# Performance work log

Measured on AMD Instinct MI355X. Metric: run time of the kernel, lower is better.

## Reference

```python
import jax, jax.numpy as jnp
import numpy as np

B, S, HID = 4, 1024, 1024
NH = 32
HD = HID // NH  # 32, equals NH (required by the module's bias broadcast)
MAX_POS = 1024
EPS = 1e-12


def setup_inputs() -> dict:
    key = jax.random.key(0)
    ks = jax.random.split(key, 12)
    sc = 0.02
    return {
        "hidden_states": jax.random.normal(ks[0], (B, S, HID), jnp.float32),
        "Wq": jax.random.normal(ks[1], (HID, HID), jnp.float32) * sc,
        "bq": jnp.zeros((HID,), jnp.float32),
        "Wk": jax.random.normal(ks[2], (HID, HID), jnp.float32) * sc,
        "bk": jnp.zeros((HID,), jnp.float32),
        "Wv": jax.random.normal(ks[3], (HID, HID), jnp.float32) * sc,
        "bv": jnp.zeros((HID,), jnp.float32),
        "Wo": jax.random.normal(ks[4], (HID, HID), jnp.float32) * sc,
        "bo": jnp.zeros((HID,), jnp.float32),
        "ln_gamma": jnp.ones((HID,), jnp.float32),
        "ln_beta": jnp.zeros((HID,), jnp.float32),
        "dist_emb": jax.random.normal(ks[5], (2 * MAX_POS - 1, HD), jnp.float32) * sc,
    }


def reference(hidden_states, Wq, bq, Wk, bk, Wv, bv, Wo, bo, ln_gamma, ln_beta, dist_emb):
    b, s, hid = hidden_states.shape
    # QKV projections (torch Linear: x @ W.T + b), split heads -> (b, h, s, d)
    def split_heads(x):
        return x.reshape(b, s, NH, HD).transpose(0, 2, 1, 3)
    q = split_heads(hidden_states @ Wq.T + bq)
    k = split_heads(hidden_states @ Wk.T + bk)
    v = split_heads(hidden_states @ Wv.T + bv)

    # Relative position bias: rel in [0, 2*max_pos-2], emb -> (s, s, HD)
    pos = jnp.arange(s)
    rel = pos[:, None] - pos[None, :] + (MAX_POS - 1)  # (s, s)
    # permute(0,3,1,2): (b, HD, s, s); identical across batch -> broadcast.
    # Broadcasts against (b, NH, s, s) since HD == NH (module requirement).
    bias = dist_emb[rel].transpose(2, 0, 1)  # (HD, s, s)

    scores = jnp.einsum("bhqd,bhkd->bhqk", q, k)  # (b, h, s, s)
    scores = (scores + bias[None]) / np.sqrt(HD)  # bias added BEFORE scaling, as in source
    probs = jax.nn.softmax(scores, axis=-1)

    ctx = jnp.einsum("bhqk,bhkd->bhqd", probs, v)
    ctx = ctx.transpose(0, 2, 1, 3).reshape(b, s, hid)
    attn_out = ctx @ Wo.T + bo

    # residual + LayerNorm
    x = attn_out + hidden_states
    mu = jnp.mean(x, axis=-1, keepdims=True)
    var = jnp.mean(jnp.square(x - mu), axis=-1, keepdims=True)
    out = (x - mu) / jnp.sqrt(var + EPS) * ln_gamma + ln_beta
    return out, probs
```

## Files before the change

### kernel.cpp

```cpp
#include <hip/hip_runtime.h>
#include <math.h>

#define BB 4
#define SS 1024
#define HIDD 1024
#define NH 32
#define HD 32
#define RS 0.17677669529663687f

#define BM 128
#define BN 128
#define BK 16

__global__ __launch_bounds__(256) void gemm_qkv(
    const float* __restrict__ X,
    const float* __restrict__ W0, const float* __restrict__ W1, const float* __restrict__ W2,
    const float* __restrict__ c0, const float* __restrict__ c1, const float* __restrict__ c2,
    float* __restrict__ O0, float* __restrict__ O1, float* __restrict__ O2)
{
    const int zi = blockIdx.z;
    const float* Wm = (zi == 0) ? W0 : (zi == 1 ? W1 : W2);
    const float* bm = (zi == 0) ? c0 : (zi == 1 ? c1 : c2);
    float* Om       = (zi == 0) ? O0 : (zi == 1 ? O1 : O2);

    const int i0 = blockIdx.x * BM;
    const int j0 = blockIdx.y * BN;
    const int tid = threadIdx.x;
    const int tx = tid & 15, ty = tid >> 4;
    const int m0 = tx * 8, n0 = ty * 8;

    __shared__ float As[BK][BM + 4];
    __shared__ float Bs[BK][BN + 4];

    float acc[8][8] = {};

    for (int k0 = 0; k0 < 1024; k0 += BK) {
        #pragma unroll
        for (int f0 = 0; f0 < 2; ++f0) {
            int f = tid + f0 * 256;
            int r = f >> 2;
            int c4 = (f & 3) * 4;
            float4 a = *(const float4*)&X[(size_t)(i0 + r) * 1024 + k0 + c4];
            As[c4 + 0][r] = a.x; As[c4 + 1][r] = a.y;
            As[c4 + 2][r] = a.z; As[c4 + 3][r] = a.w;
            float4 w = *(const float4*)&Wm[(size_t)(j0 + r) * 1024 + k0 + c4];
            Bs[c4 + 0][r] = w.x; Bs[c4 + 1][r] = w.y;
            Bs[c4 + 2][r] = w.z; Bs[c4 + 3][r] = w.w;
        }
        __syncthreads();
        #pragma unroll
        for (int k = 0; k < BK; ++k) {
            float ar[8], br[8];
            *(float4*)&ar[0] = *(const float4*)&As[k][m0];
            *(float4*)&ar[4] = *(const float4*)&As[k][m0 + 4];
            *(float4*)&br[0] = *(const float4*)&Bs[k][n0];
            *(float4*)&br[4] = *(const float4*)&Bs[k][n0 + 4];
            #pragma unroll
            for (int mm = 0; mm < 8; ++mm)
                #pragma unroll
                for (int nn = 0; nn < 8; ++nn)
                    acc[mm][nn] += ar[mm] * br[nn];
        }
        __syncthreads();
    }

    #pragma unroll
    for (int mm = 0; mm < 8; ++mm) {
        int i = i0 + m0 + mm;
        int bi = i >> 10, si = i & 1023;
        #pragma unroll
        for (int nn4 = 0; nn4 < 8; nn4 += 4) {
            int j = j0 + n0 + nn4;
            int h = j >> 5, d = j & 31;
            float4 o;
            o.x = acc[mm][nn4 + 0] + bm[j + 0];
            o.y = acc[mm][nn4 + 1] + bm[j + 1];
            o.z = acc[mm][nn4 + 2] + bm[j + 2];
            o.w = acc[mm][nn4 + 3] + bm[j + 3];
            *(float4*)&Om[(((size_t)bi * NH + h) * SS + si) * HD + d] = o;
        }
    }
}

__global__ __launch_bounds__(256) void gemm_out(
    const float* __restrict__ X, const float* __restrict__ Wm,
    const float* __restrict__ bm, const float* __restrict__ res,
    float* __restrict__ Om)
{
    const int i0 = blockIdx.x * BM;
    const int j0 = blockIdx.y * BN;
    const int tid = threadIdx.x;
    const int tx = tid & 15, ty = tid >> 4;
    const int m0 = tx * 8, n0 = ty * 8;

    __shared__ float As[BK][BM + 4];
    __shared__ float Bs[BK][BN + 4];

    float acc[8][8] = {};

    for (int k0 = 0; k0 < 1024; k0 += BK) {
        #pragma unroll
        for (int f0 = 0; f0 < 2; ++f0) {
            int f = tid + f0 * 256;
            int r = f >> 2;
            int c4 = (f & 3) * 4;
            float4 a = *(const float4*)&X[(size_t)(i0 + r) * 1024 + k0 + c4];
            As[c4 + 0][r] = a.x; As[c4 + 1][r] = a.y;
            As[c4 + 2][r] = a.z; As[c4 + 3][r] = a.w;
            float4 w = *(const float4*)&Wm[(size_t)(j0 + r) * 1024 + k0 + c4];
            Bs[c4 + 0][r] = w.x; Bs[c4 + 1][r] = w.y;
            Bs[c4 + 2][r] = w.z; Bs[c4 + 3][r] = w.w;
        }
        __syncthreads();
        #pragma unroll
        for (int k = 0; k < BK; ++k) {
            float ar[8], br[8];
            *(float4*)&ar[0] = *(const float4*)&As[k][m0];
            *(float4*)&ar[4] = *(const float4*)&As[k][m0 + 4];
            *(float4*)&br[0] = *(const float4*)&Bs[k][n0];
            *(float4*)&br[4] = *(const float4*)&Bs[k][n0 + 4];
            #pragma unroll
            for (int mm = 0; mm < 8; ++mm)
                #pragma unroll
                for (int nn = 0; nn < 8; ++nn)
                    acc[mm][nn] += ar[mm] * br[nn];
        }
        __syncthreads();
    }

    #pragma unroll
    for (int mm = 0; mm < 8; ++mm) {
        int i = i0 + m0 + mm;
        #pragma unroll
        for (int nn4 = 0; nn4 < 8; nn4 += 4) {
            int j = j0 + n0 + nn4;
            float4 r4 = *(const float4*)&res[(size_t)i * 1024 + j];
            float4 o;
            o.x = acc[mm][nn4 + 0] + bm[j + 0] + r4.x;
            o.y = acc[mm][nn4 + 1] + bm[j + 1] + r4.y;
            o.z = acc[mm][nn4 + 2] + bm[j + 2] + r4.z;
            o.w = acc[mm][nn4 + 3] + bm[j + 3] + r4.w;
            *(float4*)&Om[(size_t)i * 1024 + j] = o;
        }
    }
}

__global__ __launch_bounds__(256) void attn_kernel(
    const float* __restrict__ Q, const float* __restrict__ K,
    const float* __restrict__ V, const float* __restrict__ dist,
    float* __restrict__ probs, float* __restrict__ ctx)
{
    const int tile = blockIdx.x;
    const int h = blockIdx.y;
    const int b = blockIdx.z;
    const int tid = threadIdx.x;
    const int r0 = tile * 512;
    const size_t bh = (size_t)(b * NH + h);
    const float* Qh = Q + bh * SS * HD;
    const float* Kh = K + bh * SS * HD;
    const float* Vh = V + bh * SS * HD;
    float* Ph = probs + bh * SS * SS;

    __shared__ float Kt[512 * HD];
    __shared__ float Vt[512 * HD];
    __shared__ float dl[1536];

    for (int t = tid; t < 1535; t += 256)
        dl[t] = dist[(size_t)(r0 + t) * HD + h];

    for (int f = tid; f < 4096; f += 256) {
        ((float4*)Kt)[f] = ((const float4*)Kh)[f];
        ((float4*)Vt)[f] = ((const float4*)Kh)[f + 4096];
    }

    float q1[32], q2[32];
    #pragma unroll
    for (int d4 = 0; d4 < 8; ++d4) {
        float4 a = ((const float4*)(Qh + (size_t)(r0 + tid) * HD))[d4];
        q1[d4 * 4 + 0] = a.x; q1[d4 * 4 + 1] = a.y;
        q1[d4 * 4 + 2] = a.z; q1[d4 * 4 + 3] = a.w;
        float4 c = ((const float4*)(Qh + (size_t)(r0 + 256 + tid) * HD))[d4];
        q2[d4 * 4 + 0] = c.x; q2[d4 * 4 + 1] = c.y;
        q2[d4 * 4 + 2] = c.z; q2[d4 * 4 + 3] = c.w;
    }
    __syncthreads();

    float m1 = -1e30f, l1 = 0.f, m2 = -1e30f, l2 = 0.f;
    #pragma unroll 1
    for (int ht = 0; ht < 2; ++ht) {
        const float* KT = ht ? Vt : Kt;
        const int jbase = ht * 512;
        #pragma unroll 2
        for (int j = 0; j < 512; ++j) {
            const float* kr = KT + j * HD;
            float a1 = 0.f, a2 = 0.f;
            #pragma unroll
            for (int d4 = 0; d4 < 8; ++d4) {
                float4 kv = ((const float4*)kr)[d4];
                a1 += q1[d4*4+0]*kv.x + q1[d4*4+1]*kv.y + q1[d4*4+2]*kv.z + q1[d4*4+3]*kv.w;
                a2 += q2[d4*4+0]*kv.x + q2[d4*4+1]*kv.y + q2[d4*4+2]*kv.z + q2[d4*4+3]*kv.w;
            }
            int jg = jbase + j;
            float s1 = (a1 + dl[tid + 1023 - jg]) * RS;
            float s2 = (a2 + dl[tid + 1279 - jg]) * RS;
            if (s1 > m1) { l1 *= __expf(m1 - s1); m1 = s1; }
            l1 += __expf(s1 - m1);
            if (s2 > m2) { l2 *= __expf(m2 - s2); m2 = s2; }
            l2 += __expf(s2 - m2);
        }
    }
    const float rl1 = 1.f / l1, rl2 = 1.f / l2;

    float c1[32] = {}, c2[32] = {};

    #pragma unroll 1
    for (int jt = 0; jt < 2; ++jt) {
        __syncthreads();
        for (int f = tid; f < 4096; f += 256) {
            if (jt) ((float4*)Kt)[f] = ((const float4*)(Kh + (size_t)jt * 512 * HD))[f];
            ((float4*)Vt)[f] = ((const float4*)(Vh + (size_t)jt * 512 * HD))[f];
        }
        __syncthreads();

        #pragma unroll 1
        for (int jj = 0; jj < 512; jj += 4) {
            float pa1[4], pa2[4];
            #pragma unroll
            for (int u = 0; u < 4; ++u) {
                const float* kr = Kt + (jj + u) * HD;
                float a1 = 0.f, a2 = 0.f;
                #pragma unroll
                for (int d4 = 0; d4 < 8; ++d4) {
                    float4 kv = ((const float4*)kr)[d4];
                    a1 += q1[d4*4+0]*kv.x + q1[d4*4+1]*kv.y + q1[d4*4+2]*kv.z + q1[d4*4+3]*kv.w;
                    a2 += q2[d4*4+0]*kv.x + q2[d4*4+1]*kv.y + q2[d4*4+2]*kv.z + q2[d4*4+3]*kv.w;
                }
                int jg = jt * 512 + jj + u;
                float s1 = (a1 + dl[tid + 1023 - jg]) * RS;
                float s2 = (a2 + dl[tid + 1279 - jg]) * RS;
                pa1[u] = __expf(s1 - m1) * rl1;
                pa2[u] = __expf(s2 - m2) * rl2;
            }
            int jg0 = jt * 512 + jj;
            *(float4*)&Ph[(size_t)(r0 + tid) * SS + jg0] =
                make_float4(pa1[0], pa1[1], pa1[2], pa1[3]);
            *(float4*)&Ph[(size_t)(r0 + 256 + tid) * SS + jg0] =
                make_float4(pa2[0], pa2[1], pa2[2], pa2[3]);
            #pragma unroll
            for (int u = 0; u < 4; ++u) {
                const float* vr = Vt + (jj + u) * HD;
                #pragma unroll
                for (int d4 = 0; d4 < 8; ++d4) {
                    float4 vv = ((const float4*)vr)[d4];
                    c1[d4*4+0] += pa1[u]*vv.x; c1[d4*4+1] += pa1[u]*vv.y;
                    c1[d4*4+2] += pa1[u]*vv.z; c1[d4*4+3] += pa1[u]*vv.w;
                    c2[d4*4+0] += pa2[u]*vv.x; c2[d4*4+1] += pa2[u]*vv.y;
                    c2[d4*4+2] += pa2[u]*vv.z; c2[d4*4+3] += pa2[u]*vv.w;
                }
            }
        }
    }

    float* cp1 = ctx + (size_t)(b * SS + r0 + tid) * HIDD + h * HD;
    float* cp2 = ctx + (size_t)(b * SS + r0 + 256 + tid) * HIDD + h * HD;
    #pragma unroll
    for (int d4 = 0; d4 < 8; ++d4) {
        ((float4*)cp1)[d4] = make_float4(c1[d4*4], c1[d4*4+1], c1[d4*4+2], c1[d4*4+3]);
        ((float4*)cp2)[d4] = make_float4(c2[d4*4], c2[d4*4+1], c2[d4*4+2], c2[d4*4+3]);
    }
}

__global__ __launch_bounds__(256) void ln_kernel(
    const float* __restrict__ X, const float* __restrict__ gamma,
    const float* __restrict__ beta, float* __restrict__ out)
{
    const int row = blockIdx.x;
    const int tid = threadIdx.x;
    const float* xr = X + (size_t)row * 1024;
    float4 x = *(const float4*)&xr[tid * 4];
    float s = x.x + x.y + x.z + x.w;
    float q = x.x*x.x + x.y*x.y + x.z*x.z + x.w*x.w;
    #pragma unroll
    for (int off = 32; off; off >>= 1) {
        s += __shfl_xor(s, off);
        q += __shfl_xor(q, off);
    }
    __shared__ float ps[4], pq[4];
    int wid = tid >> 6, lane = tid & 63;
    if (lane == 0) { ps[wid] = s; pq[wid] = q; }
    __syncthreads();
    s = ps[0] + ps[1] + ps[2] + ps[3];
    q = pq[0] + pq[1] + pq[2] + pq[3];
    float mu = s * (1.0f / 1024.0f);
    float var = q * (1.0f / 1024.0f) - mu * mu;
    float rstd = 1.0f / sqrtf(var + 1e-12f);
    float4 g = *(const float4*)&gamma[tid * 4];
    float4 bt = *(const float4*)&beta[tid * 4];
    float4 o;
    o.x = (x.x - mu) * rstd * g.x + bt.x;
    o.y = (x.y - mu) * rstd * g.y + bt.y;
    o.z = (x.z - mu) * rstd * g.z + bt.z;
    o.w = (x.w - mu) * rstd * g.w + bt.w;
    *(float4*)&out[(size_t)row * 1024 + tid * 4] = o;
}

extern "C" void kernel_launch(void* const* d_in, const int* in_sizes, int n_in,
                              void* d_out, int out_size, void* d_ws, size_t ws_size,
                              hipStream_t stream)
{
    const float* hid  = (const float*)d_in[0];
    const float* Wq   = (const float*)d_in[1];
    const float* bq   = (const float*)d_in[2];
    const float* Wk   = (const float*)d_in[3];
    const float* bk   = (const float*)d_in[4];
    const float* Wv   = (const float*)d_in[5];
    const float* bvv  = (const float*)d_in[6];
    const float* Wo   = (const float*)d_in[7];
    const float* bo   = (const float*)d_in[8];
    const float* lng  = (const float*)d_in[9];
    const float* lnb  = (const float*)d_in[10];
    const float* dist = (const float*)d_in[11];

    float* out   = (float*)d_out;
    float* probs = out + (size_t)BB * SS * HIDD;

    const size_t QN = (size_t)BB * NH * SS * HD;
    float* ws   = (float*)d_ws;
    float* Qb   = ws;
    float* Kb   = ws + QN;
    float* Vb   = ws + 2 * QN;
    float* ctxb = ws + 3 * QN;
    float* xres = ws;

    gemm_qkv<<<dim3(32, 8, 3), 256, 0, stream>>>(hid, Wq, Wk, Wv, bq, bk, bvv, Qb, Kb, Vb);
    attn_kernel<<<dim3(2, NH, BB), 256, 0, stream>>>(Qb, Kb, Vb, dist, probs, ctxb);
    gemm_out<<<dim3(32, 8), 256, 0, stream>>>(ctxb, Wo, bo, hid, xres);
    ln_kernel<<<4096, 256, 0, stream>>>(xres, lng, lnb, out);
}
```

Measured before the change: 1.850 ms.

## Retile attention into 32-row query blocks with swizzled LDS and cooperative softmax

The attention kernel is rebuilt so each block handles 32 query rows instead of 512. Each thread computes a 2x8 score micro-tile over 128-key chunks staged in XOR-swizzled LDS. Row max and sum statistics, and the context accumulators, are combined with cross-lane shuffles, which raises the grid from 256 to 4096 blocks and lets each CU hold more blocks at once. Separately, both GEMMs change the per-thread row and column mapping to two strided groups of 4, to reduce LDS bank conflicts on the fragment reads. The costs are extra shuffle reductions over 64 context values per thread and re-staging K and V for every query block.

```diff
diff --git a/kernel.cpp b/kernel.cpp
--- a/kernel.cpp
+++ b/kernel.cpp
@@ -27,7 +27,8 @@
     const int j0 = blockIdx.y * BN;
     const int tid = threadIdx.x;
     const int tx = tid & 15, ty = tid >> 4;
-    const int m0 = tx * 8, n0 = ty * 8;
+    const int ra = tx * 4, rb = 64 + tx * 4;
+    const int ca = ty * 4, cb = 64 + ty * 4;
 
     __shared__ float As[BK][BM + 4];
     __shared__ float Bs[BK][BN + 4];
@@ -51,10 +52,10 @@
         #pragma unroll
         for (int k = 0; k < BK; ++k) {
             float ar[8], br[8];
-            *(float4*)&ar[0] = *(const float4*)&As[k][m0];
-            *(float4*)&ar[4] = *(const float4*)&As[k][m0 + 4];
-            *(float4*)&br[0] = *(const float4*)&Bs[k][n0];
-            *(float4*)&br[4] = *(const float4*)&Bs[k][n0 + 4];
+            *(float4*)&ar[0] = *(const float4*)&As[k][ra];
+            *(float4*)&ar[4] = *(const float4*)&As[k][rb];
+            *(float4*)&br[0] = *(const float4*)&Bs[k][ca];
+            *(float4*)&br[4] = *(const float4*)&Bs[k][cb];
             #pragma unroll
             for (int mm = 0; mm < 8; ++mm)
                 #pragma unroll
@@ -66,17 +67,17 @@
 
     #pragma unroll
     for (int mm = 0; mm < 8; ++mm) {
-        int i = i0 + m0 + mm;
+        int i = i0 + ((mm < 4) ? (ra + mm) : (rb + mm - 4));
         int bi = i >> 10, si = i & 1023;
         #pragma unroll
-        for (int nn4 = 0; nn4 < 8; nn4 += 4) {
-            int j = j0 + n0 + nn4;
+        for (int g = 0; g < 2; ++g) {
+            int j = j0 + (g == 0 ? ca : cb);
             int h = j >> 5, d = j & 31;
             float4 o;
-            o.x = acc[mm][nn4 + 0] + bm[j + 0];
-            o.y = acc[mm][nn4 + 1] + bm[j + 1];
-            o.z = acc[mm][nn4 + 2] + bm[j + 2];
-            o.w = acc[mm][nn4 + 3] + bm[j + 3];
+            o.x = acc[mm][g*4 + 0] + bm[j + 0];
+            o.y = acc[mm][g*4 + 1] + bm[j + 1];
+            o.z = acc[mm][g*4 + 2] + bm[j + 2];
+            o.w = acc[mm][g*4 + 3] + bm[j + 3];
             *(float4*)&Om[(((size_t)bi * NH + h) * SS + si) * HD + d] = o;
         }
     }
@@ -91,7 +92,8 @@
     const int j0 = blockIdx.y * BN;
     const int tid = threadIdx.x;
     const int tx = tid & 15, ty = tid >> 4;
-    const int m0 = tx * 8, n0 = ty * 8;
+    const int ra = tx * 4, rb = 64 + tx * 4;
+    const int ca = ty * 4, cb = 64 + ty * 4;
 
     __shared__ float As[BK][BM + 4];
     __shared__ float Bs[BK][BN + 4];
@@ -115,10 +117,10 @@
         #pragma unroll
         for (int k = 0; k < BK; ++k) {
             float ar[8], br[8];
-            *(float4*)&ar[0] = *(const float4*)&As[k][m0];
-            *(float4*)&ar[4] = *(const float4*)&As[k][m0 + 4];
-            *(float4*)&br[0] = *(const float4*)&Bs[k][n0];
-            *(float4*)&br[4] = *(const float4*)&Bs[k][n0 + 4];
+            *(float4*)&ar[0] = *(const float4*)&As[k][ra];
+            *(float4*)&ar[4] = *(const float4*)&As[k][rb];
+            *(float4*)&br[0] = *(const float4*)&Bs[k][ca];
+            *(float4*)&br[4] = *(const float4*)&Bs[k][cb];
             #pragma unroll
             for (int mm = 0; mm < 8; ++mm)
                 #pragma unroll
@@ -130,143 +132,180 @@
 
     #pragma unroll
     for (int mm = 0; mm < 8; ++mm) {
-        int i = i0 + m0 + mm;
-        #pragma unroll
-        for (int nn4 = 0; nn4 < 8; nn4 += 4) {
-            int j = j0 + n0 + nn4;
+        int i = i0 + ((mm < 4) ? (ra + mm) : (rb + mm - 4));
+        #pragma unroll
+        for (int g = 0; g < 2; ++g) {
+            int j = j0 + (g == 0 ? ca : cb);
             float4 r4 = *(const float4*)&res[(size_t)i * 1024 + j];
             float4 o;
-            o.x = acc[mm][nn4 + 0] + bm[j + 0] + r4.x;
-            o.y = acc[mm][nn4 + 1] + bm[j + 1] + r4.y;
-            o.z = acc[mm][nn4 + 2] + bm[j + 2] + r4.z;
-            o.w = acc[mm][nn4 + 3] + bm[j + 3] + r4.w;
+            o.x = acc[mm][g*4 + 0] + bm[j + 0] + r4.x;
+            o.y = acc[mm][g*4 + 1] + bm[j + 1] + r4.y;
+            o.z = acc[mm][g*4 + 2] + bm[j + 2] + r4.z;
+            o.w = acc[mm][g*4 + 3] + bm[j + 3] + r4.w;
             *(float4*)&Om[(size_t)i * 1024 + j] = o;
         }
     }
 }
 
-__global__ __launch_bounds__(256) void attn_kernel(
+__global__ __launch_bounds__(256, 3) void attn_kernel(
     const float* __restrict__ Q, const float* __restrict__ K,
     const float* __restrict__ V, const float* __restrict__ dist,
     float* __restrict__ probs, float* __restrict__ ctx)
 {
-    const int tile = blockIdx.x;
-    const int h = blockIdx.y;
-    const int b = blockIdx.z;
+    const int q0 = blockIdx.x * 32;
+    const int h  = blockIdx.y;
+    const int b  = blockIdx.z;
     const int tid = threadIdx.x;
-    const int r0 = tile * 512;
+    const int rg = tid >> 4;
+    const int cg = tid & 15;
     const size_t bh = (size_t)(b * NH + h);
     const float* Qh = Q + bh * SS * HD;
     const float* Kh = K + bh * SS * HD;
     const float* Vh = V + bh * SS * HD;
     float* Ph = probs + bh * SS * SS;
 
-    __shared__ float Kt[512 * HD];
-    __shared__ float Vt[512 * HD];
-    __shared__ float dl[1536];
-
-    for (int t = tid; t < 1535; t += 256)
-        dl[t] = dist[(size_t)(r0 + t) * HD + h];
-
-    for (int f = tid; f < 4096; f += 256) {
-        ((float4*)Kt)[f] = ((const float4*)Kh)[f];
-        ((float4*)Vt)[f] = ((const float4*)Kh)[f + 4096];
-    }
-
-    float q1[32], q2[32];
-    #pragma unroll
-    for (int d4 = 0; d4 < 8; ++d4) {
-        float4 a = ((const float4*)(Qh + (size_t)(r0 + tid) * HD))[d4];
-        q1[d4 * 4 + 0] = a.x; q1[d4 * 4 + 1] = a.y;
-        q1[d4 * 4 + 2] = a.z; q1[d4 * 4 + 3] = a.w;
-        float4 c = ((const float4*)(Qh + (size_t)(r0 + 256 + tid) * HD))[d4];
-        q2[d4 * 4 + 0] = c.x; q2[d4 * 4 + 1] = c.y;
-        q2[d4 * 4 + 2] = c.z; q2[d4 * 4 + 3] = c.w;
-    }
-    __syncthreads();
-
-    float m1 = -1e30f, l1 = 0.f, m2 = -1e30f, l2 = 0.f;
-    #pragma unroll 1
-    for (int ht = 0; ht < 2; ++ht) {
-        const float* KT = ht ? Vt : Kt;
-        const int jbase = ht * 512;
-        #pragma unroll 2
-        for (int j = 0; j < 512; ++j) {
-            const float* kr = KT + j * HD;
-            float a1 = 0.f, a2 = 0.f;
+    __shared__ float Qs[32 * 32];
+    __shared__ float Kt[128 * 32];
+    __shared__ float Vt[128 * 32];
+    __shared__ float dl[1055];
+
+    {
+        int r = tid >> 3, d4 = tid & 7;
+        float4 qv = *(const float4*)&Qh[(size_t)(q0 + r) * HD + d4 * 4];
+        *(float4*)&Qs[r * 32 + ((d4 ^ (r & 7)) << 2)] = qv;
+        for (int t = tid; t < 1055; t += 256)
+            dl[t] = dist[(size_t)(q0 + t) * HD + h];
+    }
+
+    auto stage = [&](float* lds, const float* src, int c0) {
+        #pragma unroll
+        for (int it = 0; it < 4; ++it) {
+            int f4 = tid + it * 256;
+            int c = f4 >> 3;
+            int d4 = f4 & 7;
+            float4 v = *(const float4*)&src[(size_t)(c0 + c) * HD + d4 * 4];
+            *(float4*)&lds[c * 32 + ((d4 ^ ((c >> 3) & 7)) << 2)] = v;
+        }
+    };
+
+    const int r0l = rg * 2, r1l = rg * 2 + 1;
+
+    auto qk_tile = [&](const float* Kb, int c0, float sv[2][8]) {
+        #pragma unroll
+        for (int i = 0; i < 2; ++i)
+            #pragma unroll
+            for (int u = 0; u < 8; ++u) sv[i][u] = 0.f;
+        #pragma unroll
+        for (int d4 = 0; d4 < 8; ++d4) {
+            float4 qa = *(const float4*)&Qs[r0l * 32 + ((d4 ^ (r0l & 7)) << 2)];
+            float4 qb = *(const float4*)&Qs[r1l * 32 + ((d4 ^ (r1l & 7)) << 2)];
+            #pragma unroll
+            for (int u = 0; u < 8; ++u) {
+                const int cl = ((u >> 2) << 6) + (cg << 2) + (u & 3);
+                float4 kv = *(const float4*)&Kb[cl * 32 + ((d4 ^ ((cl >> 3) & 7)) << 2)];
+                sv[0][u] += qa.x*kv.x + qa.y*kv.y + qa.z*kv.z + qa.w*kv.w;
+                sv[1][u] += qb.x*kv.x + qb.y*kv.y + qb.z*kv.z + qb.w*kv.w;
+            }
+        }
+        #pragma unroll
+        for (int i = 0; i < 2; ++i)
+            #pragma unroll
+            for (int u = 0; u < 8; ++u) {
+                const int cl = ((u >> 2) << 6) + (cg << 2) + (u & 3);
+                sv[i][u] = (sv[i][u] + dl[r0l + i + 1023 - c0 - cl]) * RS;
+            }
+    };
+
+    float mr[2] = {-1e30f, -1e30f}, lr[2] = {0.f, 0.f};
+
+    auto ml_update = [&](float sv[2][8]) {
+        #pragma unroll
+        for (int i = 0; i < 2; ++i) {
+            float tm = sv[i][0];
+            #pragma unroll
+            for (int u = 1; u < 8; ++u) tm = fmaxf(tm, sv[i][u]);
+            float M = fmaxf(mr[i], tm);
+            lr[i] *= __expf(mr[i] - M);
+            mr[i] = M;
+            #pragma unroll
+            for (int u = 0; u < 8; ++u) lr[i] += __expf(sv[i][u] - M);
+        }
+    };
+
+    for (int t = 0; t < 8; t += 2) {
+        __syncthreads();
+        stage(Kt, Kh, t * 128);
+        stage(Vt, Kh, (t + 1) * 128);
+        __syncthreads();
+        float sv[2][8];
+        qk_tile(Kt, t * 128, sv);       ml_update(sv);
+        qk_tile(Vt, (t + 1) * 128, sv); ml_update(sv);
+    }
+
+    #pragma unroll
+    for (int off = 1; off < 16; off <<= 1) {
+        #pragma unroll
+        for (int i = 0; i < 2; ++i) {
+            float mo = __shfl_xor(mr[i], off);
+            float lo = __shfl_xor(lr[i], off);
+            float M = fmaxf(mr[i], mo);
+            lr[i] = lr[i] * __expf(mr[i] - M) + lo * __expf(mo - M);
+            mr[i] = M;
+        }
+    }
+    const float rl0 = 1.f / lr[0], rl1 = 1.f / lr[1];
+
+    float ca0[32] = {}, ca1[32] = {};
+    for (int t = 0; t < 8; ++t) {
+        const int c0 = t * 128;
+        __syncthreads();
+        stage(Kt, Kh, c0);
+        stage(Vt, Vh, c0);
+        __syncthreads();
+        float sv[2][8];
+        qk_tile(Kt, c0, sv);
+        float p0[8], p1[8];
+        #pragma unroll
+        for (int u = 0; u < 8; ++u) {
+            p0[u] = __expf(sv[0][u] - mr[0]) * rl0;
+            p1[u] = __expf(sv[1][u] - mr[1]) * rl1;
+        }
+        #pragma unroll
+        for (int u4 = 0; u4 < 2; ++u4) {
+            int cbase = c0 + u4 * 64 + (cg << 2);
+            *(float4*)&Ph[(size_t)(q0 + r0l) * SS + cbase] =
+                make_float4(p0[u4*4+0], p0[u4*4+1], p0[u4*4+2], p0[u4*4+3]);
+            *(float4*)&Ph[(size_t)(q0 + r1l) * SS + cbase] =
+                make_float4(p1[u4*4+0], p1[u4*4+1], p1[u4*4+2], p1[u4*4+3]);
+        }
+        #pragma unroll
+        for (int u = 0; u < 8; ++u) {
+            const int cl = ((u >> 2) << 6) + (cg << 2) + (u & 3);
+            const float pa = p0[u], pb = p1[u];
             #pragma unroll
             for (int d4 = 0; d4 < 8; ++d4) {
-                float4 kv = ((const float4*)kr)[d4];
-                a1 += q1[d4*4+0]*kv.x + q1[d4*4+1]*kv.y + q1[d4*4+2]*kv.z + q1[d4*4+3]*kv.w;
-                a2 += q2[d4*4+0]*kv.x + q2[d4*4+1]*kv.y + q2[d4*4+2]*kv.z + q2[d4*4+3]*kv.w;
+                float4 vv = *(const float4*)&Vt[cl * 32 + ((d4 ^ ((cl >> 3) & 7)) << 2)];
+                ca0[d4*4+0] += pa*vv.x; ca0[d4*4+1] += pa*vv.y;
+                ca0[d4*4+2] += pa*vv.z; ca0[d4*4+3] += pa*vv.w;
+                ca1[d4*4+0] += pb*vv.x; ca1[d4*4+1] += pb*vv.y;
+                ca1[d4*4+2] += pb*vv.z; ca1[d4*4+3] += pb*vv.w;
             }
-            int jg = jbase + j;
-            float s1 = (a1 + dl[tid + 1023 - jg]) * RS;
-            float s2 = (a2 + dl[tid + 1279 - jg]) * RS;
-            if (s1 > m1) { l1 *= __expf(m1 - s1); m1 = s1; }
-            l1 += __expf(s1 - m1);
-            if (s2 > m2) { l2 *= __expf(m2 - s2); m2 = s2; }
-            l2 += __expf(s2 - m2);
-        }
-    }
-    const float rl1 = 1.f / l1, rl2 = 1.f / l2;
-
-    float c1[32] = {}, c2[32] = {};
-
-    #pragma unroll 1
-    for (int jt = 0; jt < 2; ++jt) {
-        __syncthreads();
-        for (int f = tid; f < 4096; f += 256) {
-            if (jt) ((float4*)Kt)[f] = ((const float4*)(Kh + (size_t)jt * 512 * HD))[f];
-            ((float4*)Vt)[f] = ((const float4*)(Vh + (size_t)jt * 512 * HD))[f];
-        }
-        __syncthreads();
-
-        #pragma unroll 1
-        for (int jj = 0; jj < 512; jj += 4) {
-            float pa1[4], pa2[4];
-            #pragma unroll
-            for (int u = 0; u < 4; ++u) {
-                const float* kr = Kt + (jj + u) * HD;
-                float a1 = 0.f, a2 = 0.f;
-                #pragma unroll
-                for (int d4 = 0; d4 < 8; ++d4) {
-                    float4 kv = ((const float4*)kr)[d4];
-                    a1 += q1[d4*4+0]*kv.x + q1[d4*4+1]*kv.y + q1[d4*4+2]*kv.z + q1[d4*4+3]*kv.w;
-                    a2 += q2[d4*4+0]*kv.x + q2[d4*4+1]*kv.y + q2[d4*4+2]*kv.z + q2[d4*4+3]*kv.w;
-                }
-                int jg = jt * 512 + jj + u;
-                float s1 = (a1 + dl[tid + 1023 - jg]) * RS;
-                float s2 = (a2 + dl[tid + 1279 - jg]) * RS;
-                pa1[u] = __expf(s1 - m1) * rl1;
-                pa2[u] = __expf(s2 - m2) * rl2;
-            }
-            int jg0 = jt * 512 + jj;
-            *(float4*)&Ph[(size_t)(r0 + tid) * SS + jg0] =
-                make_float4(pa1[0], pa1[1], pa1[2], pa1[3]);
-            *(float4*)&Ph[(size_t)(r0 + 256 + tid) * SS + jg0] =
-                make_float4(pa2[0], pa2[1], pa2[2], pa2[3]);
-            #pragma unroll
-            for (int u = 0; u < 4; ++u) {
-                const float* vr = Vt + (jj + u) * HD;
-                #pragma unroll
-                for (int d4 = 0; d4 < 8; ++d4) {
-                    float4 vv = ((const float4*)vr)[d4];
-                    c1[d4*4+0] += pa1[u]*vv.x; c1[d4*4+1] += pa1[u]*vv.y;
-                    c1[d4*4+2] += pa1[u]*vv.z; c1[d4*4+3] += pa1[u]*vv.w;
-                    c2[d4*4+0] += pa2[u]*vv.x; c2[d4*4+1] += pa2[u]*vv.y;
-                    c2[d4*4+2] += pa2[u]*vv.z; c2[d4*4+3] += pa2[u]*vv.w;
-                }
-            }
-        }
-    }
-
-    float* cp1 = ctx + (size_t)(b * SS + r0 + tid) * HIDD + h * HD;
-    float* cp2 = ctx + (size_t)(b * SS + r0 + 256 + tid) * HIDD + h * HD;
-    #pragma unroll
-    for (int d4 = 0; d4 < 8; ++d4) {
-        ((float4*)cp1)[d4] = make_float4(c1[d4*4], c1[d4*4+1], c1[d4*4+2], c1[d4*4+3]);
-        ((float4*)cp2)[d4] = make_float4(c2[d4*4], c2[d4*4+1], c2[d4*4+2], c2[d4*4+3]);
+        }
+    }
+
+    #pragma unroll
+    for (int off = 1; off < 16; off <<= 1) {
+        #pragma unroll
+        for (int d = 0; d < 32; ++d) {
+            ca0[d] += __shfl_xor(ca0[d], off);
+            ca1[d] += __shfl_xor(ca1[d], off);
+        }
+    }
+    {
+        float* cp0 = ctx + ((size_t)(b * SS + q0 + r0l)) * HIDD + h * HD;
+        float* cp1 = ctx + ((size_t)(b * SS + q0 + r1l)) * HIDD + h * HD;
+        *(float2*)&cp0[cg * 2] = make_float2(ca0[cg*2], ca0[cg*2+1]);
+        *(float2*)&cp1[cg * 2] = make_float2(ca1[cg*2], ca1[cg*2+1]);
     }
 }
 
@@ -333,7 +372,7 @@
     float* xres = ws;
 
     gemm_qkv<<<dim3(32, 8, 3), 256, 0, stream>>>(hid, Wq, Wk, Wv, bq, bk, bvv, Qb, Kb, Vb);
-    attn_kernel<<<dim3(2, NH, BB), 256, 0, stream>>>(Qb, Kb, Vb, dist, probs, ctxb);
+    attn_kernel<<<dim3(32, NH, BB), 256, 0, stream>>>(Qb, Kb, Vb, dist, probs, ctxb);
     gemm_out<<<dim3(32, 8), 256, 0, stream>>>(ctxb, Wo, bo, hid, xres);
     ln_kernel<<<4096, 256, 0, stream>>>(xres, lng, lnb, out);
 }
```

Result: slower. 3.292 ms (+77.9%).
